# Kernel tuning notes

Measured on AMD Instinct MI355X. Metric: run time of the kernel, lower is better.

## Reference

```python
import jax, jax.numpy as jnp
import numpy as np

N = 50000        # nodes
E = 800000       # edges
D_IN = 512       # input_shape
PROJ = 256       # proj_dim
H = 4            # num_heads
C = 32           # hidden_channels
HC = H * C
NUM_LABELS = 10
SLOPE = 0.2      # GATv2 LeakyReLU negative slope


def _glorot(key, shape):
    fan_in = shape[-1]
    return jax.random.normal(key, shape, jnp.float32) / jnp.sqrt(jnp.float32(fan_in))


def setup_inputs() -> dict:
    key = jax.random.key(0)
    ks = jax.random.split(key, 16)
    inp = {}
    inp["x"] = jax.random.normal(ks[0], (N, D_IN), jnp.float32)
    inp["edge_index"] = jax.random.randint(ks[1], (2, E), 0, N, dtype=jnp.int64)
    # projection Linear
    inp["W_proj"] = _glorot(ks[2], (PROJ, D_IN)); inp["b_proj"] = jnp.zeros((PROJ,), jnp.float32)
    # GATv2 layer 1: lin_l, lin_r, att, bias
    inp["Wl1"] = _glorot(ks[3], (HC, PROJ)); inp["bl1"] = jnp.zeros((HC,), jnp.float32)
    inp["Wr1"] = _glorot(ks[4], (HC, PROJ)); inp["br1"] = jnp.zeros((HC,), jnp.float32)
    inp["att1"] = _glorot(ks[5], (H, C)); inp["bias1"] = jnp.zeros((HC,), jnp.float32)
    # GATv2 layer 2
    inp["Wl2"] = _glorot(ks[6], (HC, HC)); inp["bl2"] = jnp.zeros((HC,), jnp.float32)
    inp["Wr2"] = _glorot(ks[7], (HC, HC)); inp["br2"] = jnp.zeros((HC,), jnp.float32)
    inp["att2"] = _glorot(ks[8], (H, C)); inp["bias2"] = jnp.zeros((HC,), jnp.float32)
    # head MLP
    inp["W1"] = _glorot(ks[9], (C, HC)); inp["b1"] = jnp.zeros((C,), jnp.float32)
    inp["W2"] = _glorot(ks[10], (NUM_LABELS, C)); inp["b2"] = jnp.zeros((NUM_LABELS,), jnp.float32)
    return inp


def _gatv2(x, src, dst, Wl, bl, Wr, br, att, bias):
    # x: [N, F_in]; src/dst: [E]. PyG GATv2Conv, concat=True, no self-loops, eval (no dropout).
    xl = (x @ Wl.T + bl).reshape(N, H, C)   # source transform
    xr = (x @ Wr.T + br).reshape(N, H, C)   # target transform
    e = jax.nn.leaky_relu(xl[src] + xr[dst], negative_slope=SLOPE)  # [E,H,C]
    logit = jnp.einsum('ehc,hc->eh', e, att)                        # [E,H]
    # segment softmax over incoming edges of each destination node
    m = jax.ops.segment_max(logit, dst, num_segments=N)             # [N,H]
    m = jnp.where(jnp.isfinite(m), m, jnp.float32(0))               # empty segments -> 0
    p = jnp.exp(logit - m[dst])                                     # [E,H]
    s = jax.ops.segment_sum(p, dst, num_segments=N)                 # [N,H]
    alpha = p / (s[dst] + jnp.float32(1e-16))                       # [E,H]
    out = jax.ops.segment_sum(xl[src] * alpha[:, :, None], dst, num_segments=N)  # [N,H,C]
    return out.reshape(N, HC) + bias


def reference(x, edge_index, W_proj, b_proj, Wl1, bl1, Wr1, br1, att1, bias1,
              Wl2, bl2, Wr2, br2, att2, bias2, W1, b1, W2, b2):
    src, dst = edge_index[0], edge_index[1]
    h = jax.nn.elu(x @ W_proj.T + b_proj)
    h = jax.nn.elu(_gatv2(h, src, dst, Wl1, bl1, Wr1, br1, att1, bias1))
    h = jax.nn.elu(_gatv2(h, src, dst, Wl2, bl2, Wr2, br2, att2, bias2))
    h = jax.nn.elu(h @ W1.T + b1)
    return h @ W2.T + b2
```

## Files before the change

### kernel.cpp

```cpp
#include <hip/hip_runtime.h>
#include <cstdint>
#include <cstddef>

constexpr int NN = 50000;
constexpr int NE = 800000;

typedef _Float16 half8 __attribute__((ext_vector_type(8)));
typedef _Float16 half4v __attribute__((ext_vector_type(4)));
typedef _Float16 half2v __attribute__((ext_vector_type(2)));
typedef float f32x16 __attribute__((ext_vector_type(16)));
typedef unsigned short ushort_t;

__device__ inline ushort_t f2h(float f) {
  _Float16 h = (_Float16)f;
  return __builtin_bit_cast(ushort_t, h);
}

#if __has_builtin(__builtin_amdgcn_fdot2)
__device__ inline float fdot2(half2v a, half2v b, float c) {
  return __builtin_amdgcn_fdot2(a, b, c, false);
}
#else
__device__ inline float fdot2(half2v a, half2v b, float c) {
  return c + (float)a[0] * (float)b[0] + (float)a[1] * (float)b[1];
}
#endif

__global__ void k_wconv(const float* __restrict__ W, ushort_t* __restrict__ Bh,
                        int M, int K, int total) {
  int idx = blockIdx.x * 256 + threadIdx.x;
  if (idx >= total) return;
  int j = idx & 7;
  int l = (idx >> 3) & 63;
  int blk = idx >> 9;
  int nKB = K >> 4;
  int cb = blk / nKB, kb = blk - cb * nKB;
  int col = cb * 32 + (l & 31);
  int k = kb * 16 + ((l >> 5) & 1) * 8 + j;
  float v = (col < M) ? W[(size_t)col * K + k] : 0.f;
  Bh[idx] = f2h(v);
}

template<int ACT, int OUTMODE, int BKT, int AFP16, int NCB>
__global__ __launch_bounds__(512) void gemm_mfma(const void* __restrict__ Av,
    const ushort_t* __restrict__ Bh,
    const float* __restrict__ bias, const float* __restrict__ bias2,
    float* __restrict__ C, ushort_t* __restrict__ C16a,
    ushort_t* __restrict__ C16b, int N, int M, int K)
{
  constexpr int NKK = BKT / 16;
  __shared__ ushort_t Ah[2][2 * NKK * 512];
  const int t = threadIdx.x;
  const int lane = t & 63;
  const int wid = t >> 6;
  const int wr = wid >> 2;
  const int wc = wid & 3;
  const int row0 = blockIdx.x * 64;
  const int col0 = blockIdx.y * (128 * NCB);
  const int nKB = K >> 4;
  const int nK = K / BKT;
  const int cb0 = (col0 >> 5) + wc * NCB;

  int s_r, s_k, sb0, sb1 = 0;
  bool ok0 = false, ok1 = false;
  if constexpr (!AFP16) {
    s_r = t >> 4; s_k = (t & 15) * 4;
    sb0 = (s_k >> 4) * 512 + (s_r + 32 * ((s_k >> 3) & 1)) * 8 + (s_k & 7);
    sb1 = sb0 + NKK * 512;
    ok0 = (row0 + s_r) < N;
    ok1 = (row0 + s_r + 32) < N;
  } else if constexpr (BKT == 64) {
    s_r = t >> 3; s_k = (t & 7) * 8;
    sb0 = ((s_r >> 5) * NKK + (s_k >> 4)) * 512 +
          ((s_r & 31) + 32 * ((s_k >> 3) & 1)) * 8;
    ok0 = (row0 + s_r) < N;
  } else {
    s_r = t >> 3; s_k = (t & 7) * 4;
    sb0 = ((s_r >> 5) * NKK + (s_k >> 4)) * 512 +
          ((s_r & 31) + 32 * ((s_k >> 3) & 1)) * 8 + (s_k & 7);
    ok0 = (row0 + s_r) < N;
  }
  const float*    ap0 = (const float*)Av + (size_t)(row0 + s_r) * K + s_k;
  const float*    ap1 = (const float*)Av + (size_t)(row0 + s_r + 32) * K + s_k;
  const ushort_t* aph = (const ushort_t*)Av + (size_t)(row0 + s_r) * K + s_k;

  f32x16 acc0 = {}, acc1 = {};
  float4 f0 = make_float4(0, 0, 0, 0), f1 = make_float4(0, 0, 0, 0);
  half8 h8 = {};
  half4v h4 = {};

  auto aload = [&](int ks) {
    if constexpr (!AFP16) {
      f0 = make_float4(0, 0, 0, 0);
      f1 = make_float4(0, 0, 0, 0);
      if (ok0) f0 = *(const float4*)(ap0 + (size_t)ks * BKT);
      if (ok1) f1 = *(const float4*)(ap1 + (size_t)ks * BKT);
    } else if constexpr (BKT == 64) {
      half8 z = {};
      h8 = ok0 ? *(const half8*)(aph + (size_t)ks * BKT) : z;
    } else {
      half4v z = {};
      h4 = ok0 ? *(const half4v*)(aph + (size_t)ks * BKT) : z;
    }
  };
  auto stage_write = [&](int buf) {
    if constexpr (!AFP16) {
      half4v a, b;
      a[0] = (_Float16)f0.x; a[1] = (_Float16)f0.y;
      a[2] = (_Float16)f0.z; a[3] = (_Float16)f0.w;
      b[0] = (_Float16)f1.x; b[1] = (_Float16)f1.y;
      b[2] = (_Float16)f1.z; b[3] = (_Float16)f1.w;
      *(half4v*)&Ah[buf][sb0] = a;
      *(half4v*)&Ah[buf][sb1] = b;
    } else if constexpr (BKT == 64) {
      *(half8*)&Ah[buf][sb0] = h8;
    } else {
      *(half4v*)&Ah[buf][sb0] = h4;
    }
  };

  aload(0);
  stage_write(0);
  __syncthreads();

  for (int ks = 0; ks < nK; ++ks) {
    const int cur = ks & 1;
    const int nxt = cur ^ 1;
    const bool have_next = (ks + 1 < nK);
    if (have_next) aload(ks + 1);

    #pragma unroll
    for (int kk = 0; kk < NKK; ++kk) {
      const int kbg = ks * NKK + kk;
      half8 ah = *(const half8*)&Ah[cur][(wr * NKK + kk) * 512 + lane * 8];
      const size_t bo0 = ((size_t)(cb0 * nKB + kbg) * 64 + lane) * 8;
      half8 bh0 = *(const half8*)(Bh + bo0);
      acc0 = __builtin_amdgcn_mfma_f32_32x32x16_f16(ah, bh0, acc0, 0, 0, 0);
      if constexpr (NCB == 2) {
        const size_t bo1 = ((size_t)((cb0 + 1) * nKB + kbg) * 64 + lane) * 8;
        half8 bh1 = *(const half8*)(Bh + bo1);
        acc1 = __builtin_amdgcn_mfma_f32_32x32x16_f16(ah, bh1, acc1, 0, 0, 0);
      }
    }

    if (have_next) stage_write(nxt);
    __syncthreads();
  }

  auto epi = [&](const f32x16& acc, int cb) {
    int cc = cb * 32 + (lane & 31);
    float bv;
    if constexpr (OUTMODE == 3) bv = (cc < 128) ? bias[cc] : bias2[cc - 128];
    else                        bv = (cc < M) ? bias[cc] : 0.f;
    #pragma unroll
    for (int r = 0; r < 16; ++r) {
      int rr = row0 + wr * 32 + (r & 3) + 8 * (r >> 2) + 4 * (lane >> 5);
      if (rr < N && cc < M) {
        float v = acc[r] + bv;
        if (ACT) v = v > 0.f ? v : (__expf(v) - 1.f);
        if constexpr (OUTMODE == 0)      C[(size_t)rr * M + cc] = v;
        else if constexpr (OUTMODE == 1) C16a[(size_t)rr * M + cc] = f2h(v);
        else {
          if (cc < 128) C16a[(size_t)rr * 128 + cc] = f2h(v);
          else          C16b[(size_t)rr * 128 + (cc - 128)] = f2h(v);
        }
      }
    }
  };
  epi(acc0, cb0);
  if constexpr (NCB == 2) epi(acc1, cb0 + 1);
}

__global__ void k_degrank(const int* __restrict__ ei, int* __restrict__ deg,
                          int* __restrict__ rank) {
  int e = blockIdx.x * 256 + threadIdx.x;
  if (e >= NE) return;
  int d = ei[NE + e];
  rank[e] = atomicAdd(&deg[d], 1);
}

__global__ __launch_bounds__(256) void k_scan1(const int* __restrict__ deg,
    int* __restrict__ rowstart, int* __restrict__ blocksum) {
  __shared__ int sm[256];
  int b = blockIdx.x, t = threadIdx.x;
  int i = b * 256 + t;
  int v = (i < NN) ? deg[i] : 0;
  sm[t] = v;
  __syncthreads();
  #pragma unroll
  for (int off = 1; off < 256; off <<= 1) {
    int u = (t >= off) ? sm[t - off] : 0;
    __syncthreads();
    sm[t] += u;
    __syncthreads();
  }
  if (i < NN) rowstart[i + 1] = sm[t];
  if (t == 255) blocksum[b] = sm[255];
}

__global__ __launch_bounds__(256) void k_scan2(int* __restrict__ blocksum, int nb) {
  __shared__ int sm[256];
  int t = threadIdx.x;
  int v = (t < nb) ? blocksum[t] : 0;
  sm[t] = v;
  __syncthreads();
  #pragma unroll
  for (int off = 1; off < 256; off <<= 1) {
    int u = (t >= off) ? sm[t - off] : 0;
    __syncthreads();
    sm[t] += u;
    __syncthreads();
  }
  if (t < nb) blocksum[t] = (t == 0) ? 0 : sm[t - 1];
}

__global__ __launch_bounds__(256) void k_scan3(int* __restrict__ rowstart,
    const int* __restrict__ blocksum) {
  int b = blockIdx.x, t = threadIdx.x;
  int i = b * 256 + t;
  if (i == 0) rowstart[0] = 0;
  if (i < NN) rowstart[i + 1] += blocksum[b];
}

__global__ void k_scatter(const int* __restrict__ ei, const int* __restrict__ rowstart,
                          const int* __restrict__ rank, int* __restrict__ srcp) {
  int e = blockIdx.x * 256 + threadIdx.x;
  if (e >= NE) return;
  int d = ei[NE + e];
  srcp[rowstart[d] + rank[e]] = ei[e];
}

__global__ __launch_bounds__(256) void k_gat(const ushort_t* __restrict__ xl,
    const ushort_t* __restrict__ xr, const int* __restrict__ srcp,
    const int* __restrict__ rowstart, const float* __restrict__ att,
    const float* __restrict__ bias, ushort_t* __restrict__ out)
{
  const int g = threadIdx.x >> 5;
  const int c = threadIdx.x & 31;
  const int n = blockIdx.x * 8 + g;
  const int r0 = rowstart[n], r1 = rowstart[n + 1];
  half4v xrh = *(const half4v*)(xr + (size_t)n * 128 + 4 * c);
  const half2v xr01 = {xrh[0], xrh[1]};
  const half2v xr23 = {xrh[2], xrh[3]};
  const float4 atv = *(const float4*)(att + 4 * c);
  const half2v at01 = {(_Float16)atv.x, (_Float16)atv.y};
  const half2v at23 = {(_Float16)atv.z, (_Float16)atv.w};
  const half2v k02 = {(_Float16)0.2f, (_Float16)0.2f};

  float m = -1e30f, ssum = 0.f;
  float a0 = 0.f, a1 = 0.f, a2 = 0.f, a3 = 0.f;

  auto lg = [&](int s, float4& xs) -> float {
    half4v hv = *(const half4v*)(xl + (size_t)s * 128 + 4 * c);
    xs.x = (float)hv[0]; xs.y = (float)hv[1];
    xs.z = (float)hv[2]; xs.w = (float)hv[3];
    half2v u01 = half2v{hv[0], hv[1]} + xr01;
    half2v u23 = half2v{hv[2], hv[3]} + xr23;
    u01 = __builtin_elementwise_max(u01, u01 * k02);
    u23 = __builtin_elementwise_max(u23, u23 * k02);
    float l = fdot2(u01, at01, fdot2(u23, at23, 0.f));
    l += __shfl_xor(l, 1);
    l += __shfl_xor(l, 2);
    l += __shfl_xor(l, 4);
    return l;
  };

  int j = r0;
  for (; j + 8 <= r1; j += 8) {
    int s0 = srcp[j],     s1 = srcp[j + 1], s2 = srcp[j + 2], s3 = srcp[j + 3];
    int s4 = srcp[j + 4], s5 = srcp[j + 5], s6 = srcp[j + 6], s7 = srcp[j + 7];
    float4 x0, x1, x2, x3, x4, x5, x6, x7;
    float l0 = lg(s0, x0), l1 = lg(s1, x1), l2 = lg(s2, x2), l3 = lg(s3, x3);
    float l4 = lg(s4, x4), l5 = lg(s5, x5), l6 = lg(s6, x6), l7 = lg(s7, x7);
    float mloc = fmaxf(fmaxf(fmaxf(l0, l1), fmaxf(l2, l3)),
                       fmaxf(fmaxf(l4, l5), fmaxf(l6, l7)));
    float mn = fmaxf(m, mloc);
    float sc = __expf(m - mn);
    float p0 = __expf(l0 - mn), p1 = __expf(l1 - mn);
    float p2 = __expf(l2 - mn), p3 = __expf(l3 - mn);
    float p4 = __expf(l4 - mn), p5 = __expf(l5 - mn);
    float p6 = __expf(l6 - mn), p7 = __expf(l7 - mn);
    ssum = ssum * sc + (((p0 + p1) + (p2 + p3)) + ((p4 + p5) + (p6 + p7)));
    a0 = a0 * sc + (((p0 * x0.x + p1 * x1.x) + (p2 * x2.x + p3 * x3.x)) +
                    ((p4 * x4.x + p5 * x5.x) + (p6 * x6.x + p7 * x7.x)));
    a1 = a1 * sc + (((p0 * x0.y + p1 * x1.y) + (p2 * x2.y + p3 * x3.y)) +
                    ((p4 * x4.y + p5 * x5.y) + (p6 * x6.y + p7 * x7.y)));
    a2 = a2 * sc + (((p0 * x0.z + p1 * x1.z) + (p2 * x2.z + p3 * x3.z)) +
                    ((p4 * x4.z + p5 * x5.z) + (p6 * x6.z + p7 * x7.z)));
    a3 = a3 * sc + (((p0 * x0.w + p1 * x1.w) + (p2 * x2.w + p3 * x3.w)) +
                    ((p4 * x4.w + p5 * x5.w) + (p6 * x6.w + p7 * x7.w)));
    m = mn;
  }
  for (; j + 4 <= r1; j += 4) {
    int s0 = srcp[j], s1 = srcp[j + 1], s2 = srcp[j + 2], s3 = srcp[j + 3];
    float4 x0, x1, x2, x3;
    float l0 = lg(s0, x0), l1 = lg(s1, x1), l2 = lg(s2, x2), l3 = lg(s3, x3);
    float mloc = fmaxf(fmaxf(l0, l1), fmaxf(l2, l3));
    float mn = fmaxf(m, mloc);
    float sc = __expf(m - mn);
    float p0 = __expf(l0 - mn), p1 = __expf(l1 - mn);
    float p2 = __expf(l2 - mn), p3 = __expf(l3 - mn);
    ssum = ssum * sc + ((p0 + p1) + (p2 + p3));
    a0 = a0 * sc + (p0 * x0.x + p1 * x1.x) + (p2 * x2.x + p3 * x3.x);
    a1 = a1 * sc + (p0 * x0.y + p1 * x1.y) + (p2 * x2.y + p3 * x3.y);
    a2 = a2 * sc + (p0 * x0.z + p1 * x1.z) + (p2 * x2.z + p3 * x3.z);
    a3 = a3 * sc + (p0 * x0.w + p1 * x1.w) + (p2 * x2.w + p3 * x3.w);
    m = mn;
  }
  for (; j < r1; ++j) {
    float4 xs;
    float l = lg(srcp[j], xs);
    float mn = fmaxf(m, l);
    float sc = __expf(m - mn);
    float p = __expf(l - mn);
    ssum = ssum * sc + p;
    a0 = a0 * sc + p * xs.x;
    a1 = a1 * sc + p * xs.y;
    a2 = a2 * sc + p * xs.z;
    a3 = a3 * sc + p * xs.w;
    m = mn;
  }

  const float4 bv = *(const float4*)(bias + 4 * c);
  float rinv = 1.f / (ssum + 1e-16f);
  float o0 = a0 * rinv + bv.x;
  float o1 = a1 * rinv + bv.y;
  float o2 = a2 * rinv + bv.z;
  float o3 = a3 * rinv + bv.w;
  o0 = o0 > 0.f ? o0 : (__expf(o0) - 1.f);
  o1 = o1 > 0.f ? o1 : (__expf(o1) - 1.f);
  o2 = o2 > 0.f ? o2 : (__expf(o2) - 1.f);
  o3 = o3 > 0.f ? o3 : (__expf(o3) - 1.f);
  half4v ov;
  ov[0] = (_Float16)o0; ov[1] = (_Float16)o1;
  ov[2] = (_Float16)o2; ov[3] = (_Float16)o3;
  *(half4v*)(out + (size_t)n * 128 + 4 * c) = ov;
}

__global__ void k_report_ws(float* out, int out_size, float wsz) {
  int i = blockIdx.x * 256 + threadIdx.x;
  if (i < out_size) out[i] = (i == 0) ? wsz : 0.f;
}

extern "C" void kernel_launch(void* const* d_in, const int* in_sizes, int n_in,
                              void* d_out, int out_size, void* d_ws, size_t ws_size,
                              hipStream_t stream)
{
  const float* x    = (const float*)d_in[0];
  const int*   ei   = (const int*)d_in[1];
  const float* Wp   = (const float*)d_in[2];  const float* bp    = (const float*)d_in[3];
  const float* Wl1  = (const float*)d_in[4];  const float* bl1   = (const float*)d_in[5];
  const float* Wr1  = (const float*)d_in[6];  const float* br1   = (const float*)d_in[7];
  const float* att1 = (const float*)d_in[8];  const float* bias1 = (const float*)d_in[9];
  const float* Wl2  = (const float*)d_in[10]; const float* bl2   = (const float*)d_in[11];
  const float* Wr2  = (const float*)d_in[12]; const float* br2   = (const float*)d_in[13];
  const float* att2 = (const float*)d_in[14]; const float* bias2 = (const float*)d_in[15];
  const float* W1   = (const float*)d_in[16]; const float* b1    = (const float*)d_in[17];
  const float* W2   = (const float*)d_in[18]; const float* b2    = (const float*)d_in[19];
  float* out = (float*)d_out;

  constexpr size_t NEED = 122300000;
  if (ws_size < NEED) {
    k_report_ws<<<(out_size + 255) / 256, 256, 0, stream>>>(out, out_size, (float)ws_size);
    return;
  }
  char* ws = (char*)d_ws;
  ushort_t* h0h   = (ushort_t*)(ws + 0);
  ushort_t* h1h   = h0h;
  ushort_t* h2h   = (ushort_t*)(ws + 25600000);
  ushort_t* xlh   = (ushort_t*)(ws + 51200000);
  ushort_t* xrh   = (ushort_t*)(ws + 76800000);
  ushort_t* h3h   = (ushort_t*)(ws + 102400000);
  ushort_t* wb    = (ushort_t*)(ws + 108800000);
  int*      srcp  = (int*)(ws + 115200000);
  int*      rank  = (int*)(ws + 118400000);
  int*      deg   = (int*)(ws + 121600000);
  int*      rowst = (int*)(ws + 122000000);
  int*      bsum  = (int*)(ws + 122250000);

  ushort_t* Wph  = wb;
  ushort_t* WB1h = wb + 131072;
  ushort_t* WB2h = wb + 196608;
  ushort_t* W1h  = wb + 229376;
  ushort_t* W2h  = wb + 233472;

  hipMemsetAsync(deg, 0, NN * sizeof(int), stream);

  k_wconv<<<(131072+255)/256, 256, 0, stream>>>(Wp,  Wph,          256, 512, 131072);
  k_wconv<<<(32768+255)/256,  256, 0, stream>>>(Wl1, WB1h,         128, 256, 32768);
  k_wconv<<<(32768+255)/256,  256, 0, stream>>>(Wr1, WB1h + 32768, 128, 256, 32768);
  k_wconv<<<(16384+255)/256,  256, 0, stream>>>(Wl2, WB2h,         128, 128, 16384);
  k_wconv<<<(16384+255)/256,  256, 0, stream>>>(Wr2, WB2h + 16384, 128, 128, 16384);
  k_wconv<<<(4096+255)/256,   256, 0, stream>>>(W1,  W1h,          32,  128, 4096);
  k_wconv<<<(1024+255)/256,   256, 0, stream>>>(W2,  W2h,          10,  32,  1024);

  constexpr int NB = (NN + 255) / 256;
  k_degrank<<<(NE+255)/256, 256, 0, stream>>>(ei, deg, rank);
  k_scan1  <<<NB, 256, 0, stream>>>(deg, rowst, bsum);
  k_scan2  <<<1, 256, 0, stream>>>(bsum, NB);
  k_scan3  <<<NB, 256, 0, stream>>>(rowst, bsum);
  k_scatter<<<(NE+255)/256, 256, 0, stream>>>(ei, rowst, rank, srcp);

  constexpr int GX = (NN + 63) / 64;

  gemm_mfma<1,1,64,0,2><<<dim3(GX, 1), 512, 0, stream>>>(
      x, Wph, bp, nullptr, nullptr, h0h, nullptr, NN, 256, 512);

  gemm_mfma<0,3,64,1,2><<<dim3(GX, 1), 512, 0, stream>>>(
      h0h, WB1h, bl1, br1, nullptr, xlh, xrh, NN, 256, 256);
  k_gat<<<NN/8, 256, 0, stream>>>(xlh, xrh, srcp, rowst, att1, bias1, h1h);

  gemm_mfma<0,3,64,1,2><<<dim3(GX, 1), 512, 0, stream>>>(
      h1h, WB2h, bl2, br2, nullptr, xlh, xrh, NN, 256, 128);
  k_gat<<<NN/8, 256, 0, stream>>>(xlh, xrh, srcp, rowst, att2, bias2, h2h);

  gemm_mfma<1,1,64,1,1><<<dim3(GX, 1), 512, 0, stream>>>(
      h2h, W1h, b1, nullptr, nullptr, h3h, nullptr, NN, 32, 128);
  gemm_mfma<0,0,32,1,1><<<dim3(GX, 1), 512, 0, stream>>>(
      h3h, W2h, b2, nullptr, out, nullptr, nullptr, NN, 10, 32);
}
```

Baseline: 265.4 us.

## Fuse input projection GEMM with layer-1 lin_l/lin_r GEMM via shared memory

Adds a kernel that computes the ELU projection of x for a 64-row tile, keeps the fp16 result in shared memory in MFMA fragment layout, and immediately multiplies it by the concatenated layer-1 left/right weights. This removes the global write and reread of the 50000x256 intermediate and one kernel launch. The trade-off is extra shared memory per block (about 48KB), which may lower occupancy. The second GEMM also reads its weights straight from global memory without double buffering.

```diff
diff --git a/kernel.cpp b/kernel.cpp
--- a/kernel.cpp
+++ b/kernel.cpp
@@ -39,6 +39,132 @@
   int k = kb * 16 + ((l >> 5) & 1) * 8 + j;
   float v = (col < M) ? W[(size_t)col * K + k] : 0.f;
   Bh[idx] = f2h(v);
+}
+
+__global__ __launch_bounds__(512) void gemm_proj_l1(const float* __restrict__ x,
+    const ushort_t* __restrict__ WpF, const ushort_t* __restrict__ WB1,
+    const float* __restrict__ bp, const float* __restrict__ bl1,
+    const float* __restrict__ br1, ushort_t* __restrict__ xlh,
+    ushort_t* __restrict__ xrh, int N)
+{
+  constexpr int NKK = 4;
+  constexpr int nKB1 = 32;
+  constexpr int nK1 = 8;
+  __shared__ ushort_t Ah[2][2 * NKK * 512];
+  __shared__ ushort_t H0[16384];
+  const int t = threadIdx.x;
+  const int lane = t & 63;
+  const int wid = t >> 6;
+  const int wr = wid >> 2;
+  const int wc = wid & 3;
+  const int row0 = blockIdx.x * 64;
+  const int cb0 = wc * 2;
+
+  const int s_r = t >> 4, s_k = (t & 15) * 4;
+  const int sb0 = (s_k >> 4) * 512 + (s_r + 32 * ((s_k >> 3) & 1)) * 8 + (s_k & 7);
+  const int sb1 = sb0 + NKK * 512;
+  const bool ok0 = (row0 + s_r) < N;
+  const bool ok1 = (row0 + s_r + 32) < N;
+  const float* ap0 = x + (size_t)(row0 + s_r) * 512 + s_k;
+  const float* ap1 = x + (size_t)(row0 + s_r + 32) * 512 + s_k;
+
+  f32x16 acc0 = {}, acc1 = {};
+  float4 f0 = make_float4(0, 0, 0, 0), f1 = make_float4(0, 0, 0, 0);
+
+  auto aload = [&](int ks) {
+    f0 = make_float4(0, 0, 0, 0);
+    f1 = make_float4(0, 0, 0, 0);
+    if (ok0) f0 = *(const float4*)(ap0 + (size_t)ks * 64);
+    if (ok1) f1 = *(const float4*)(ap1 + (size_t)ks * 64);
+  };
+  auto cvt4 = [](float4 f) {
+    half4v h;
+    h[0] = (_Float16)f.x; h[1] = (_Float16)f.y;
+    h[2] = (_Float16)f.z; h[3] = (_Float16)f.w;
+    return h;
+  };
+  auto stage_write = [&](int buf) {
+    *(half4v*)&Ah[buf][sb0] = cvt4(f0);
+    *(half4v*)&Ah[buf][sb1] = cvt4(f1);
+  };
+
+  aload(0);
+  stage_write(0);
+  __syncthreads();
+
+  for (int ks = 0; ks < nK1; ++ks) {
+    const int cur = ks & 1;
+    const int nxt = cur ^ 1;
+    const bool have_next = (ks + 1 < nK1);
+    if (have_next) aload(ks + 1);
+
+    #pragma unroll
+    for (int kk = 0; kk < NKK; ++kk) {
+      const int kbg = ks * NKK + kk;
+      half8 ah = *(const half8*)&Ah[cur][(wr * NKK + kk) * 512 + lane * 8];
+      const size_t bo0 = ((size_t)(cb0 * nKB1 + kbg) * 64 + lane) * 8;
+      half8 bh0 = *(const half8*)(WpF + bo0);
+      acc0 = __builtin_amdgcn_mfma_f32_32x32x16_f16(ah, bh0, acc0, 0, 0, 0);
+      const size_t bo1 = ((size_t)((cb0 + 1) * nKB1 + kbg) * 64 + lane) * 8;
+      half8 bh1 = *(const half8*)(WpF + bo1);
+      acc1 = __builtin_amdgcn_mfma_f32_32x32x16_f16(ah, bh1, acc1, 0, 0, 0);
+    }
+
+    if (have_next) stage_write(nxt);
+    __syncthreads();
+  }
+
+  {
+    int col = cb0 * 32 + (lane & 31);
+    float bv = bp[col];
+    #pragma unroll
+    for (int r = 0; r < 16; ++r) {
+      int row = wr * 32 + (r & 3) + 8 * (r >> 2) + 4 * (lane >> 5);
+      float v = acc0[r] + bv;
+      v = v > 0.f ? v : (__expf(v) - 1.f);
+      H0[((row >> 5) * 16 + (col >> 4)) * 512 +
+         ((row & 31) + 32 * ((col >> 3) & 1)) * 8 + (col & 7)] = f2h(v);
+    }
+    int col1 = col + 32;
+    float bv1 = bp[col1];
+    #pragma unroll
+    for (int r = 0; r < 16; ++r) {
+      int row = wr * 32 + (r & 3) + 8 * (r >> 2) + 4 * (lane >> 5);
+      float v = acc1[r] + bv1;
+      v = v > 0.f ? v : (__expf(v) - 1.f);
+      H0[((row >> 5) * 16 + (col1 >> 4)) * 512 +
+         ((row & 31) + 32 * ((col1 >> 3) & 1)) * 8 + (col1 & 7)] = f2h(v);
+    }
+  }
+  __syncthreads();
+
+  f32x16 acc2a = {}, acc2b = {};
+  #pragma unroll
+  for (int kk = 0; kk < 16; ++kk) {
+    half8 ah = *(const half8*)&H0[(wr * 16 + kk) * 512 + lane * 8];
+    const size_t bo0 = ((size_t)(cb0 * 16 + kk) * 64 + lane) * 8;
+    half8 bh0 = *(const half8*)(WB1 + bo0);
+    acc2a = __builtin_amdgcn_mfma_f32_32x32x16_f16(ah, bh0, acc2a, 0, 0, 0);
+    const size_t bo1 = ((size_t)((cb0 + 1) * 16 + kk) * 64 + lane) * 8;
+    half8 bh1 = *(const half8*)(WB1 + bo1);
+    acc2b = __builtin_amdgcn_mfma_f32_32x32x16_f16(ah, bh1, acc2b, 0, 0, 0);
+  }
+
+  auto epi2 = [&](const f32x16& acc, int cb) {
+    int cc = cb * 32 + (lane & 31);
+    float bv = (cc < 128) ? bl1[cc] : br1[cc - 128];
+    #pragma unroll
+    for (int r = 0; r < 16; ++r) {
+      int rr = row0 + wr * 32 + (r & 3) + 8 * (r >> 2) + 4 * (lane >> 5);
+      if (rr < N) {
+        float v = acc[r] + bv;
+        if (cc < 128) xlh[(size_t)rr * 128 + cc] = f2h(v);
+        else          xrh[(size_t)rr * 128 + (cc - 128)] = f2h(v);
+      }
+    }
+  };
+  epi2(acc2a, cb0);
+  epi2(acc2b, cb0 + 1);
 }
 
 template<int ACT, int OUTMODE, int BKT, int AFP16, int NCB>
@@ -103,15 +229,16 @@
       h4 = ok0 ? *(const half4v*)(aph + (size_t)ks * BKT) : z;
     }
   };
+  auto cvt4 = [](float4 f) {
+    half4v h;
+    h[0] = (_Float16)f.x; h[1] = (_Float16)f.y;
+    h[2] = (_Float16)f.z; h[3] = (_Float16)f.w;
+    return h;
+  };
   auto stage_write = [&](int buf) {
     if constexpr (!AFP16) {
-      half4v a, b;
-      a[0] = (_Float16)f0.x; a[1] = (_Float16)f0.y;
-      a[2] = (_Float16)f0.z; a[3] = (_Float16)f0.w;
-      b[0] = (_Float16)f1.x; b[1] = (_Float16)f1.y;
-      b[2] = (_Float16)f1.z; b[3] = (_Float16)f1.w;
-      *(half4v*)&Ah[buf][sb0] = a;
-      *(half4v*)&Ah[buf][sb1] = b;
+      *(half4v*)&Ah[buf][sb0] = cvt4(f0);
+      *(half4v*)&Ah[buf][sb1] = cvt4(f1);
     } else if constexpr (BKT == 64) {
       *(half8*)&Ah[buf][sb0] = h8;
     } else {
@@ -365,8 +492,7 @@
     return;
   }
   char* ws = (char*)d_ws;
-  ushort_t* h0h   = (ushort_t*)(ws + 0);
-  ushort_t* h1h   = h0h;
+  ushort_t* h1h   = (ushort_t*)(ws + 0);
   ushort_t* h2h   = (ushort_t*)(ws + 25600000);
   ushort_t* xlh   = (ushort_t*)(ws + 51200000);
   ushort_t* xrh   = (ushort_t*)(ws + 76800000);
@@ -403,11 +529,7 @@
 
   constexpr int GX = (NN + 63) / 64;
 
-  gemm_mfma<1,1,64,0,2><<<dim3(GX, 1), 512, 0, stream>>>(
-      x, Wph, bp, nullptr, nullptr, h0h, nullptr, NN, 256, 512);
-
-  gemm_mfma<0,3,64,1,2><<<dim3(GX, 1), 512, 0, stream>>>(
-      h0h, WB1h, bl1, br1, nullptr, xlh, xrh, NN, 256, 256);
+  gemm_proj_l1<<<GX, 512, 0, stream>>>(x, Wph, WB1h, bp, bl1, br1, xlh, xrh, NN);
   k_gat<<<NN/8, 256, 0, stream>>>(xlh, xrh, srcp, rowst, att1, bias1, h1h);
 
   gemm_mfma<0,3,64,1,2><<<dim3(GX, 1), 512, 0, stream>>>(
```

New measurement: 255.9 us. 3.6% less time.
